# Performance work log

Measured on AMD Instinct MI355X. Metric: run time of the kernel, lower is better.

The kernel has to match this reference:

```python
import jax, jax.numpy as jnp
import numpy as np

LATENT = 128   # latent_size
FDIM = 32      # feature_dim per plane
FSIZE = 512    # feature_size -> grid is (FSIZE+1)^2
HID = 256      # hidden_dim
N = 500000     # number of query points
IN_DIM = 3
G = FSIZE + 1
SDF_IN = 3 * FDIM + LATENT + IN_DIM  # 227


def setup_inputs() -> dict:
    key = jax.random.key(0)
    ks = jax.random.split(key, 6)
    x = jax.random.normal(ks[0], (N, LATENT + IN_DIM), jnp.float32)
    # 3 tri-planes, each [FDIM, G, G], init randn*0.01 as in FeaturePlanes
    P = jax.random.normal(ks[1], (3, FDIM, G, G), jnp.float32) * 0.01

    def lin(k, fan_in, fan_out):
        s = 1.0 / np.sqrt(fan_in)
        kw, kb = jax.random.split(k)
        W = jax.random.uniform(kw, (fan_in, fan_out), jnp.float32, -s, s)
        b = jax.random.uniform(kb, (fan_out,), jnp.float32, -s, s)
        return W, b

    W0, b0 = lin(ks[2], SDF_IN, HID)
    W1, b1 = lin(ks[3], HID, HID)
    W2, b2 = lin(ks[4], HID, 1)
    return dict(x=x, P=P, W0=W0, b0=b0, W1=W1, b1=b1, W2=W2, b2=b2)


def _sample_plane(plane, uv):
    """Bilinear grid_sample, align_corners=True, padding_mode='border'.
    plane: [C, G, G]; uv: [Npts, 2] with uv[:,0]->width(x), uv[:,1]->height(y).
    Returns [Npts, C]."""
    g = jnp.clip((uv + 1.0) * 0.5 * (G - 1), 0.0, G - 1)  # unnormalize + border clamp
    gx, gy = g[:, 0], g[:, 1]
    x0f, y0f = jnp.floor(gx), jnp.floor(gy)
    x0 = x0f.astype(jnp.int32)
    y0 = y0f.astype(jnp.int32)
    x1 = jnp.minimum(x0 + 1, G - 1)
    y1 = jnp.minimum(y0 + 1, G - 1)
    wx = gx - x0f
    wy = gy - y0f
    v00 = plane[:, y0, x0]  # [C, Npts]
    v01 = plane[:, y0, x1]
    v10 = plane[:, y1, x0]
    v11 = plane[:, y1, x1]
    top = v00 * (1.0 - wx) + v01 * wx
    bot = v10 * (1.0 - wx) + v11 * wx
    return (top * (1.0 - wy) + bot * wy).T  # [Npts, C]


def reference(x, P, W0, b0, W1, b1, W2, b2):
    in_latents = x[:, :LATENT]
    in_x = x[:, -3:]
    coords = jax.lax.stop_gradient(in_x)  # matches .detach() before grid_sample
    # dimension pairs (0,1), (0,2), (1,2) -> one bilinear lookup each, vmapped
    uv = jnp.stack([coords[:, [0, 1]], coords[:, [0, 2]], coords[:, [1, 2]]])  # [3,N,2]
    feats = jax.vmap(_sample_plane)(P, uv)              # [3, N, FDIM]
    feats = jnp.transpose(feats, (1, 0, 2)).reshape(x.shape[0], 3 * FDIM)
    net_in = jnp.concatenate([in_latents, in_x, feats], axis=-1)  # [N, 227]
    h = jax.nn.relu(net_in @ W0 + b0)
    h = jax.nn.relu(h @ W1 + b1)
    out = (h @ W2 + b2).squeeze(-1)  # [N]
    return out
```

## Files before the change

kernel.cpp:

```cpp
#include <hip/hip_runtime.h>
#include <stdint.h>

#define XDIM 131
#define GSZ 513
#define TROWS 64
#define SC_OFF 32768

typedef __attribute__((ext_vector_type(8))) short bf16x8;
typedef __attribute__((ext_vector_type(4))) float f32x4;
typedef unsigned int uint32;

__device__ __forceinline__ uint32 pk2bf(float a, float b) {
  uint32 r;
  asm volatile("v_cvt_pk_bf16_f32 %0, %1, %2" : "=v"(r) : "v"(a), "v"(b));
  return r;
}
__device__ __forceinline__ unsigned short f2bf(float f) {
  return (unsigned short)pk2bf(f, f);
}
__device__ __forceinline__ float bf2f(unsigned short s) {
  return __uint_as_float(((uint32)s) << 16);
}
__device__ __forceinline__ int slot16(int r) { return (r * 16) ^ (((r >> 3) & 1) << 5); }

__global__ void prep_pt(const float* __restrict__ P, unsigned short* __restrict__ Pt) {
  int i = blockIdx.x * 256 + threadIdx.x;
  const int CELLS = 3 * GSZ * GSZ;
  if (i >= CELLS) return;
  int pl = i / (GSZ * GSZ);
  int yx = i - pl * (GSZ * GSZ);
  const float* src = P + (size_t)pl * 32 * GSZ * GSZ + yx;
  const size_t GG = (size_t)GSZ * GSZ;
  uint4* dst = (uint4*)(Pt + (size_t)i * 32);
#pragma unroll
  for (int w = 0; w < 4; ++w) {
    uint4 t;
    t.x = pk2bf(src[(w * 8 + 0) * GG], src[(w * 8 + 1) * GG]);
    t.y = pk2bf(src[(w * 8 + 2) * GG], src[(w * 8 + 3) * GG]);
    t.z = pk2bf(src[(w * 8 + 4) * GG], src[(w * 8 + 5) * GG]);
    t.w = pk2bf(src[(w * 8 + 6) * GG], src[(w * 8 + 7) * GG]);
    dst[w] = t;
  }
}

__global__ void prep_w(const float* __restrict__ W0, const float* __restrict__ W1,
                       unsigned short* __restrict__ W0g, unsigned short* __restrict__ W1g) {
  int i = blockIdx.x * 256 + threadIdx.x;
  int sel = i >> 13;
  int t = i & 8191;
  int kb = t >> 10;
  int g  = (t >> 8) & 3;
  int n  = t & 255;
  float vv[8];
#pragma unroll
  for (int j = 0; j < 8; ++j) {
    int k = kb * 32 + g * 8 + j;
    float val;
    if (sel == 0) {
      int src = (k < 131) ? k : ((k >= 136 && k < 232) ? k - 5 : -1);
      val = (src >= 0) ? W0[src * 256 + n] : 0.f;
    } else {
      val = W1[k * 256 + n];
    }
    vv[j] = val;
  }
  uint4 o;
  o.x = pk2bf(vv[0], vv[1]);
  o.y = pk2bf(vv[2], vv[3]);
  o.z = pk2bf(vv[4], vv[5]);
  o.w = pk2bf(vv[6], vv[7]);
  unsigned short* dst = (sel == 0 ? W0g : W1g) + (size_t)t * 8;
  *(uint4*)dst = o;
}

__global__ __launch_bounds__(256) void k_gather(
    const float* __restrict__ x, const unsigned short* __restrict__ Pt,
    unsigned short* __restrict__ feats, int Npts)
{
  int idx = blockIdx.x * 256 + threadIdx.x;
  int p = min(idx >> 2, Npts - 1);
  int q = idx & 3;
  const float* xr = x + (size_t)p * XDIM + 128;
  float cc0 = xr[0], cc1 = xr[1], cc2 = xr[2];

  const unsigned short* pp[12];
  float w[12];
#pragma unroll
  for (int pl = 0; pl < 3; ++pl) {
    float u = (pl == 2) ? cc1 : cc0;
    float v = (pl == 0) ? cc1 : cc2;
    float gx = fminf(fmaxf((u + 1.f) * 256.f, 0.f), 512.f);
    float gy = fminf(fmaxf((v + 1.f) * 256.f, 0.f), 512.f);
    float x0f = floorf(gx), y0f = floorf(gy);
    int x0 = (int)x0f, y0 = (int)y0f;
    int x1 = min(x0 + 1, GSZ - 1), y1 = min(y0 + 1, GSZ - 1);
    float wx = gx - x0f, wy = gy - y0f;
    w[pl * 4 + 0] = (1.f - wx) * (1.f - wy);
    w[pl * 4 + 1] = wx * (1.f - wy);
    w[pl * 4 + 2] = (1.f - wx) * wy;
    w[pl * 4 + 3] = wx * wy;
    const unsigned short* pb = Pt + (size_t)pl * GSZ * GSZ * 32 + q * 8;
    pp[pl * 4 + 0] = pb + (size_t)(y0 * GSZ + x0) * 32;
    pp[pl * 4 + 1] = pb + (size_t)(y0 * GSZ + x1) * 32;
    pp[pl * 4 + 2] = pb + (size_t)(y1 * GSZ + x0) * 32;
    pp[pl * 4 + 3] = pb + (size_t)(y1 * GSZ + x1) * 32;
  }
  bf16x8 v[12];
#pragma unroll
  for (int j = 0; j < 12; ++j) v[j] = *(const bf16x8*)pp[j];

#pragma unroll
  for (int pl = 0; pl < 3; ++pl) {
    float f[8];
#pragma unroll
    for (int j = 0; j < 8; ++j) {
      f[j] = w[pl * 4 + 0] * bf2f((unsigned short)v[pl * 4 + 0][j])
           + w[pl * 4 + 1] * bf2f((unsigned short)v[pl * 4 + 1][j])
           + w[pl * 4 + 2] * bf2f((unsigned short)v[pl * 4 + 2][j])
           + w[pl * 4 + 3] * bf2f((unsigned short)v[pl * 4 + 3][j]);
    }
    uint4 fv;
    fv.x = pk2bf(f[0], f[1]);
    fv.y = pk2bf(f[2], f[3]);
    fv.z = pk2bf(f[4], f[5]);
    fv.w = pk2bf(f[6], f[7]);
    *(uint4*)(feats + (size_t)p * 96 + pl * 32 + q * 8) = fv;
  }
}

__device__ __forceinline__ void gemm64(const unsigned char* __restrict__ lds_,
                                       const unsigned short* __restrict__ Wg,
                                       int cg, int lr, int lg, f32x4 (&acc)[4][4])
{
#pragma unroll
  for (int kb = 0; kb < 8; ++kb) {
    bf16x8 a[4];
    const unsigned char* ab = lds_ + (kb * 4 + lg) * 1024;
#pragma unroll
    for (int mf = 0; mf < 4; ++mf)
      a[mf] = *(const bf16x8*)(ab + slot16(mf * 16 + lr));
    const unsigned short* wb = Wg + ((size_t)(kb * 4 + lg) * 256 + cg * 64 + lr) * 8;
    __builtin_amdgcn_s_setprio(1);
#pragma unroll
    for (int nf = 0; nf < 4; ++nf) {
      bf16x8 b = *(const bf16x8*)(wb + nf * 128);
#pragma unroll
      for (int mf = 0; mf < 4; ++mf)
        acc[mf][nf] = __builtin_amdgcn_mfma_f32_16x16x32_bf16(a[mf], b, acc[mf][nf], 0, 0, 0);
    }
    __builtin_amdgcn_s_setprio(0);
  }
}

template<int MODE>
__global__ __launch_bounds__(256, 4) void sdf_mlp(
    const float* __restrict__ x, const float* __restrict__ P,
    const unsigned short* __restrict__ Pt, const unsigned short* __restrict__ feats,
    const unsigned short* __restrict__ W0g, const unsigned short* __restrict__ W1g,
    const float* __restrict__ b0, const float* __restrict__ b1,
    const float* __restrict__ W2, const float* __restrict__ b2v,
    float* __restrict__ out, int Npts)
{
  __shared__ __align__(16) unsigned char lds[SC_OFF + 1024];

  const int tid = threadIdx.x;
  const int p0 = blockIdx.x * TROWS;
  const int lane = tid & 63, cg = tid >> 6;
  const int lr = lane & 15, lg = lane >> 4;

#pragma unroll
  for (int i = 0; i < 4; ++i) {
    int t = i * 256 + tid;
    int cb = t & 15, r = t >> 4;
    int p = min(p0 + r, Npts - 1);
    const float* src = x + (size_t)p * XDIM + cb * 8;
    uint4 v;
    v.x = pk2bf(src[0], src[1]);
    v.y = pk2bf(src[2], src[3]);
    v.z = pk2bf(src[4], src[5]);
    v.w = pk2bf(src[6], src[7]);
    *(uint4*)(lds + cb * 1024 + slot16(r)) = v;
  }
  if (tid < 64) {
    int p = min(p0 + tid, Npts - 1);
    const float* xr = x + (size_t)p * XDIM + 128;
    uint4 v;
    v.x = pk2bf(xr[0], xr[1]);
    v.y = pk2bf(xr[2], 0.f);
    v.z = 0u; v.w = 0u;
    *(uint4*)(lds + 16 * 1024 + slot16(tid)) = v;
  } else {
    uint4 z = {0u, 0u, 0u, 0u};
    ((uint4*)(lds + 29 * 1024))[tid - 64] = z;
  }

  if (MODE == 0) {
#pragma unroll
    for (int i = 0; i < 3; ++i) {
      int t = i * 256 + tid;
      int r = t & 63, j = t >> 6;
      int p = min(p0 + r, Npts - 1);
      uint4 fv = *(const uint4*)(feats + (size_t)p * 96 + j * 8);
      *(uint4*)(lds + (17 + j) * 1024 + slot16(r)) = fv;
    }
  } else {
    int p_l = tid >> 2, q = tid & 3;
    int p = min(p0 + p_l, Npts - 1);
    const float* xr = x + (size_t)p * XDIM + 128;
    float cc0 = xr[0], cc1 = xr[1], cc2 = xr[2];
#pragma unroll
    for (int pl = 0; pl < 3; ++pl) {
      float u = (pl == 2) ? cc1 : cc0;
      float v = (pl == 0) ? cc1 : cc2;
      float gx = fminf(fmaxf((u + 1.f) * 256.f, 0.f), 512.f);
      float gy = fminf(fmaxf((v + 1.f) * 256.f, 0.f), 512.f);
      float x0f = floorf(gx), y0f = floorf(gy);
      int x0 = (int)x0f, y0 = (int)y0f;
      int x1 = min(x0 + 1, GSZ - 1), y1 = min(y0 + 1, GSZ - 1);
      float wx = gx - x0f, wy = gy - y0f;
      float w00 = (1.f - wx) * (1.f - wy), w01 = wx * (1.f - wy);
      float w10 = (1.f - wx) * wy,        w11 = wx * wy;
      float f[8];
      if (MODE == 1) {
        const unsigned short* pb = Pt + (size_t)pl * GSZ * GSZ * 32 + q * 8;
        bf16x8 v00 = *(const bf16x8*)(pb + (size_t)(y0 * GSZ + x0) * 32);
        bf16x8 v01 = *(const bf16x8*)(pb + (size_t)(y0 * GSZ + x1) * 32);
        bf16x8 v10 = *(const bf16x8*)(pb + (size_t)(y1 * GSZ + x0) * 32);
        bf16x8 v11 = *(const bf16x8*)(pb + (size_t)(y1 * GSZ + x1) * 32);
#pragma unroll
        for (int j = 0; j < 8; ++j) {
          f[j] = w00 * bf2f((unsigned short)v00[j]) + w01 * bf2f((unsigned short)v01[j])
               + w10 * bf2f((unsigned short)v10[j]) + w11 * bf2f((unsigned short)v11[j]);
        }
      } else {
#pragma unroll
        for (int j = 0; j < 8; ++j) {
          const float* pc = P + (size_t)(pl * 32 + q * 8 + j) * GSZ * GSZ;
          f[j] = w00 * pc[y0 * GSZ + x0] + w01 * pc[y0 * GSZ + x1]
               + w10 * pc[y1 * GSZ + x0] + w11 * pc[y1 * GSZ + x1];
        }
      }
      uint4 fv;
      fv.x = pk2bf(f[0], f[1]);
      fv.y = pk2bf(f[2], f[3]);
      fv.z = pk2bf(f[4], f[5]);
      fv.w = pk2bf(f[6], f[7]);
      *(uint4*)(lds + (17 + pl * 4 + q) * 1024 + slot16(p_l)) = fv;
    }
  }
  __syncthreads();

  {
    f32x4 acc[4][4];
#pragma unroll
    for (int mf = 0; mf < 4; ++mf)
#pragma unroll
      for (int nf = 0; nf < 4; ++nf) acc[mf][nf] = (f32x4){0.f, 0.f, 0.f, 0.f};
    gemm64(lds, W0g, cg, lr, lg, acc);
    __syncthreads();
#pragma unroll
    for (int nf = 0; nf < 4; ++nf) {
      int col = cg * 64 + nf * 16 + lr;
      float bs = b0[col];
      unsigned char* base = lds + (col >> 3) * 1024 + (col & 7) * 2;
#pragma unroll
      for (int mf = 0; mf < 4; ++mf)
#pragma unroll
        for (int reg = 0; reg < 4; ++reg) {
          int row = mf * 16 + lg * 4 + reg;
          *(unsigned short*)(base + slot16(row)) = f2bf(fmaxf(acc[mf][nf][reg] + bs, 0.f));
        }
    }
  }
  __syncthreads();

  {
    f32x4 acc[4][4];
#pragma unroll
    for (int mf = 0; mf < 4; ++mf)
#pragma unroll
      for (int nf = 0; nf < 4; ++nf) acc[mf][nf] = (f32x4){0.f, 0.f, 0.f, 0.f};
    gemm64(lds, W1g, cg, lr, lg, acc);

    float part[4][4];
#pragma unroll
    for (int mf = 0; mf < 4; ++mf)
#pragma unroll
      for (int reg = 0; reg < 4; ++reg) part[mf][reg] = 0.f;
#pragma unroll
    for (int nf = 0; nf < 4; ++nf) {
      int col = cg * 64 + nf * 16 + lr;
      float bs = b1[col];
      float w2v = W2[col];
#pragma unroll
      for (int mf = 0; mf < 4; ++mf)
#pragma unroll
        for (int reg = 0; reg < 4; ++reg)
          part[mf][reg] += fmaxf(acc[mf][nf][reg] + bs, 0.f) * w2v;
    }
#pragma unroll
    for (int mf = 0; mf < 4; ++mf)
#pragma unroll
      for (int reg = 0; reg < 4; ++reg) {
        float v = part[mf][reg];
        v += __shfl_xor(v, 1);
        v += __shfl_xor(v, 2);
        v += __shfl_xor(v, 4);
        v += __shfl_xor(v, 8);
        part[mf][reg] = v;
      }
    if (lr == 0) {
      float* sc = (float*)(lds + SC_OFF) + cg * 64;
#pragma unroll
      for (int mf = 0; mf < 4; ++mf) {
        float4 pv;
        pv.x = part[mf][0]; pv.y = part[mf][1]; pv.z = part[mf][2]; pv.w = part[mf][3];
        *(float4*)(sc + mf * 16 + lg * 4) = pv;
      }
    }
  }
  __syncthreads();
  if (tid < 64) {
    const float* sc = (const float*)(lds + SC_OFF);
    float s = sc[tid] + sc[64 + tid] + sc[128 + tid] + sc[192 + tid] + b2v[0];
    int p = p0 + tid;
    if (p < Npts) out[p] = s;
  }
}

extern "C" void kernel_launch(void* const* d_in, const int* in_sizes, int n_in,
                              void* d_out, int out_size, void* d_ws, size_t ws_size,
                              hipStream_t stream)
{
  const float* x  = (const float*)d_in[0];
  const float* P  = (const float*)d_in[1];
  const float* W0 = (const float*)d_in[2];
  const float* b0 = (const float*)d_in[3];
  const float* W1 = (const float*)d_in[4];
  const float* b1 = (const float*)d_in[5];
  const float* W2 = (const float*)d_in[6];
  const float* b2 = (const float*)d_in[7];
  float* out = (float*)d_out;
  int Npts = in_sizes[0] / XDIM;

  const size_t PT_BYTES = (size_t)3 * GSZ * GSZ * 32 * 2;
  const size_t WG_BYTES = (size_t)8192 * 8 * 2;
  const size_t FT_BYTES = (size_t)Npts * 96 * 2;
  char* ws = (char*)d_ws;

  int mode;
  unsigned short *Ptb = nullptr, *W0g, *W1g, *ft = nullptr;
  if (ws_size >= PT_BYTES + 2 * WG_BYTES + FT_BYTES) {
    mode = 0;
    Ptb = (unsigned short*)ws;
    W0g = (unsigned short*)(ws + PT_BYTES);
    W1g = (unsigned short*)(ws + PT_BYTES + WG_BYTES);
    ft  = (unsigned short*)(ws + PT_BYTES + 2 * WG_BYTES);
  } else if (ws_size >= PT_BYTES + 2 * WG_BYTES) {
    mode = 1;
    Ptb = (unsigned short*)ws;
    W0g = (unsigned short*)(ws + PT_BYTES);
    W1g = (unsigned short*)(ws + PT_BYTES + WG_BYTES);
  } else {
    mode = 2;
    W0g = (unsigned short*)ws;
    W1g = (unsigned short*)(ws + WG_BYTES);
  }

  prep_w<<<64, 256, 0, stream>>>(W0, W1, W0g, W1g);
  if (mode != 2) prep_pt<<<(3 * GSZ * GSZ + 255) / 256, 256, 0, stream>>>(P, Ptb);
  if (mode == 0) k_gather<<<(Npts * 4 + 255) / 256, 256, 0, stream>>>(x, Ptb, ft, Npts);

  int nblk = (Npts + TROWS - 1) / TROWS;
  if (mode == 0)
    sdf_mlp<0><<<nblk, 256, 0, stream>>>(x, P, Ptb, ft, W0g, W1g, b0, b1, W2, b2, out, Npts);
  else if (mode == 1)
    sdf_mlp<1><<<nblk, 256, 0, stream>>>(x, P, Ptb, ft, W0g, W1g, b0, b1, W2, b2, out, Npts);
  else
    sdf_mlp<2><<<nblk, 256, 0, stream>>>(x, P, Ptb, ft, W0g, W1g, b0, b1, W2, b2, out, Npts);
}
```

Baseline: 363.5 us.

## Pre-pack full bf16 input tiles and run a 128-row MLP kernel

Adds a prep kernel that converts each 128-point tile (latents, coords and bilinear tri-plane features) into a bf16, LDS-swizzled 64KB tile in workspace. A new MLP kernel then streams each tile straight into LDS with global_load_lds and runs both GEMMs over 128 rows per block, with MFMA priority hints. The aim is to remove per-block fp32 x conversion and gather work from the MLP kernel and to double weight reuse per block. In exchange it needs a larger workspace (with fallbacks to the old paths) and one extra full write and read of the packed activations.

New measurement: 689.4 us. 1.9x slower.

```diff
diff --git a/kernel.cpp b/kernel.cpp
--- a/kernel.cpp
+++ b/kernel.cpp
@@ -5,6 +5,9 @@
 #define GSZ 513
 #define TROWS 64
 #define SC_OFF 32768
+#define BROWS 128
+#define KBS 2048
+#define TILE_BYTES 65536
 
 typedef __attribute__((ext_vector_type(8))) short bf16x8;
 typedef __attribute__((ext_vector_type(4))) float f32x4;
@@ -22,6 +25,12 @@
   return __uint_as_float(((uint32)s) << 16);
 }
 __device__ __forceinline__ int slot16(int r) { return (r * 16) ^ (((r >> 3) & 1) << 5); }
+
+__device__ __forceinline__ void gload_lds16(const void* g, void* l) {
+  __builtin_amdgcn_global_load_lds(
+      (const __attribute__((address_space(1))) uint32*)g,
+      (__attribute__((address_space(3))) uint32*)l, 16, 0, 0);
+}
 
 __global__ void prep_pt(const float* __restrict__ P, unsigned short* __restrict__ Pt) {
   int i = blockIdx.x * 256 + threadIdx.x;
@@ -73,18 +82,38 @@
   *(uint4*)dst = o;
 }
 
-__global__ __launch_bounds__(256) void k_gather(
+__global__ __launch_bounds__(512) void k_prep(
     const float* __restrict__ x, const unsigned short* __restrict__ Pt,
-    unsigned short* __restrict__ feats, int Npts)
-{
-  int idx = blockIdx.x * 256 + threadIdx.x;
-  int p = min(idx >> 2, Npts - 1);
-  int q = idx & 3;
-  const float* xr = x + (size_t)p * XDIM + 128;
-  float cc0 = xr[0], cc1 = xr[1], cc2 = xr[2];
-
-  const unsigned short* pp[12];
-  float w[12];
+    unsigned short* __restrict__ xall, int Npts)
+{
+  const int tid = threadIdx.x;
+  const int p_l = tid >> 2, q = tid & 3;
+  const int p = min(blockIdx.x * BROWS + p_l, Npts - 1);
+  unsigned char* dst = (unsigned char*)xall + (size_t)blockIdx.x * TILE_BYTES;
+  const float* xrow = x + (size_t)p * XDIM;
+  const int sl = slot16(p_l);
+
+#pragma unroll
+  for (int i = 0; i < 4; ++i) {
+    const float* s = xrow + q * 32 + i * 8;
+    uint4 v;
+    v.x = pk2bf(s[0], s[1]);
+    v.y = pk2bf(s[2], s[3]);
+    v.z = pk2bf(s[4], s[5]);
+    v.w = pk2bf(s[6], s[7]);
+    *(uint4*)(dst + (q * 4 + i) * KBS + sl) = v;
+  }
+  float cc0 = xrow[128], cc1 = xrow[129], cc2 = xrow[130];
+  if (q == 0) {
+    uint4 v;
+    v.x = pk2bf(cc0, cc1);
+    v.y = pk2bf(cc2, 0.f);
+    v.z = 0u; v.w = 0u;
+    *(uint4*)(dst + 16 * KBS + sl) = v;
+  } else {
+    uint4 z = {0u, 0u, 0u, 0u};
+    *(uint4*)(dst + (28 + q) * KBS + sl) = z;
+  }
 #pragma unroll
   for (int pl = 0; pl < 3; ++pl) {
     float u = (pl == 2) ? cc1 : cc0;
@@ -95,29 +124,195 @@
     int x0 = (int)x0f, y0 = (int)y0f;
     int x1 = min(x0 + 1, GSZ - 1), y1 = min(y0 + 1, GSZ - 1);
     float wx = gx - x0f, wy = gy - y0f;
-    w[pl * 4 + 0] = (1.f - wx) * (1.f - wy);
-    w[pl * 4 + 1] = wx * (1.f - wy);
-    w[pl * 4 + 2] = (1.f - wx) * wy;
-    w[pl * 4 + 3] = wx * wy;
+    float w00 = (1.f - wx) * (1.f - wy), w01 = wx * (1.f - wy);
+    float w10 = (1.f - wx) * wy,        w11 = wx * wy;
     const unsigned short* pb = Pt + (size_t)pl * GSZ * GSZ * 32 + q * 8;
-    pp[pl * 4 + 0] = pb + (size_t)(y0 * GSZ + x0) * 32;
-    pp[pl * 4 + 1] = pb + (size_t)(y0 * GSZ + x1) * 32;
-    pp[pl * 4 + 2] = pb + (size_t)(y1 * GSZ + x0) * 32;
-    pp[pl * 4 + 3] = pb + (size_t)(y1 * GSZ + x1) * 32;
-  }
-  bf16x8 v[12];
-#pragma unroll
-  for (int j = 0; j < 12; ++j) v[j] = *(const bf16x8*)pp[j];
-
+    bf16x8 v00 = *(const bf16x8*)(pb + (size_t)(y0 * GSZ + x0) * 32);
+    bf16x8 v01 = *(const bf16x8*)(pb + (size_t)(y0 * GSZ + x1) * 32);
+    bf16x8 v10 = *(const bf16x8*)(pb + (size_t)(y1 * GSZ + x0) * 32);
+    bf16x8 v11 = *(const bf16x8*)(pb + (size_t)(y1 * GSZ + x1) * 32);
+    float f[8];
+#pragma unroll
+    for (int j = 0; j < 8; ++j) {
+      f[j] = w00 * bf2f((unsigned short)v00[j]) + w01 * bf2f((unsigned short)v01[j])
+           + w10 * bf2f((unsigned short)v10[j]) + w11 * bf2f((unsigned short)v11[j]);
+    }
+    uint4 fv;
+    fv.x = pk2bf(f[0], f[1]);
+    fv.y = pk2bf(f[2], f[3]);
+    fv.z = pk2bf(f[4], f[5]);
+    fv.w = pk2bf(f[6], f[7]);
+    *(uint4*)(dst + (17 + pl * 4 + q) * KBS + sl) = fv;
+  }
+}
+
+__device__ __forceinline__ void gemm128(const unsigned char* __restrict__ lds_,
+                                        const unsigned short* __restrict__ Wg,
+                                        int cg, int lr, int lg, f32x4 (&acc)[8][4])
+{
+#pragma unroll
+  for (int kb = 0; kb < 8; ++kb) {
+    const unsigned char* ab = lds_ + (kb * 4 + lg) * KBS;
+    const unsigned short* wb = Wg + ((size_t)(kb * 4 + lg) * 256 + cg * 64 + lr) * 8;
+    bf16x8 b[4];
+#pragma unroll
+    for (int nf = 0; nf < 4; ++nf) b[nf] = *(const bf16x8*)(wb + nf * 128);
+    bf16x8 a[4];
+#pragma unroll
+    for (int mf = 0; mf < 4; ++mf) a[mf] = *(const bf16x8*)(ab + slot16(mf * 16 + lr));
+    __builtin_amdgcn_s_setprio(1);
+#pragma unroll
+    for (int nf = 0; nf < 4; ++nf)
+#pragma unroll
+      for (int mf = 0; mf < 4; ++mf)
+        acc[mf][nf] = __builtin_amdgcn_mfma_f32_16x16x32_bf16(a[mf], b[nf], acc[mf][nf], 0, 0, 0);
+    __builtin_amdgcn_s_setprio(0);
+#pragma unroll
+    for (int mf = 0; mf < 4; ++mf) a[mf] = *(const bf16x8*)(ab + slot16(64 + mf * 16 + lr));
+    __builtin_amdgcn_s_setprio(1);
+#pragma unroll
+    for (int nf = 0; nf < 4; ++nf)
+#pragma unroll
+      for (int mf = 0; mf < 4; ++mf)
+        acc[4 + mf][nf] = __builtin_amdgcn_mfma_f32_16x16x32_bf16(a[mf], b[nf], acc[4 + mf][nf], 0, 0, 0);
+    __builtin_amdgcn_s_setprio(0);
+  }
+}
+
+__global__ __launch_bounds__(256, 2) void sdf_big(
+    const unsigned short* __restrict__ xall,
+    const unsigned short* __restrict__ W0g, const unsigned short* __restrict__ W1g,
+    const float* __restrict__ b0, const float* __restrict__ b1,
+    const float* __restrict__ W2, const float* __restrict__ b2v,
+    float* __restrict__ out, int Npts)
+{
+  __shared__ __align__(16) unsigned char lds[TILE_BYTES + 2048];
+
+  const int tid = threadIdx.x;
+  const int lane = tid & 63, cg = tid >> 6;
+  const int lr = lane & 15, lg = lane >> 4;
+
+  {
+    const unsigned char* src = (const unsigned char*)xall
+                             + (size_t)blockIdx.x * TILE_BYTES + lane * 16;
+#pragma unroll
+    for (int i = 0; i < 16; ++i) {
+      int chunk = cg * 16 + i;
+      gload_lds16(src + chunk * 1024, lds + chunk * 1024);
+    }
+    asm volatile("s_waitcnt vmcnt(0)" ::: "memory");
+  }
+  __syncthreads();
+
+  {
+    f32x4 acc[8][4];
+#pragma unroll
+    for (int mh = 0; mh < 8; ++mh)
+#pragma unroll
+      for (int nf = 0; nf < 4; ++nf) acc[mh][nf] = (f32x4){0.f, 0.f, 0.f, 0.f};
+    gemm128(lds, W0g, cg, lr, lg, acc);
+    __syncthreads();
+#pragma unroll
+    for (int nf = 0; nf < 4; ++nf) {
+      int col = cg * 64 + nf * 16 + lr;
+      float bs = b0[col];
+      unsigned char* base = lds + (col >> 3) * KBS + (col & 7) * 2;
+#pragma unroll
+      for (int mh = 0; mh < 8; ++mh)
+#pragma unroll
+        for (int reg = 0; reg < 4; ++reg) {
+          int row = mh * 16 + lg * 4 + reg;
+          *(unsigned short*)(base + slot16(row)) = f2bf(fmaxf(acc[mh][nf][reg] + bs, 0.f));
+        }
+    }
+  }
+  __syncthreads();
+
+  {
+    f32x4 acc[8][4];
+#pragma unroll
+    for (int mh = 0; mh < 8; ++mh)
+#pragma unroll
+      for (int nf = 0; nf < 4; ++nf) acc[mh][nf] = (f32x4){0.f, 0.f, 0.f, 0.f};
+    gemm128(lds, W1g, cg, lr, lg, acc);
+
+    float part[8][4];
+#pragma unroll
+    for (int mh = 0; mh < 8; ++mh)
+#pragma unroll
+      for (int reg = 0; reg < 4; ++reg) part[mh][reg] = 0.f;
+#pragma unroll
+    for (int nf = 0; nf < 4; ++nf) {
+      int col = cg * 64 + nf * 16 + lr;
+      float bs = b1[col];
+      float w2v = W2[col];
+#pragma unroll
+      for (int mh = 0; mh < 8; ++mh)
+#pragma unroll
+        for (int reg = 0; reg < 4; ++reg)
+          part[mh][reg] += fmaxf(acc[mh][nf][reg] + bs, 0.f) * w2v;
+    }
+#pragma unroll
+    for (int mh = 0; mh < 8; ++mh)
+#pragma unroll
+      for (int reg = 0; reg < 4; ++reg) {
+        float v = part[mh][reg];
+        v += __shfl_xor(v, 1);
+        v += __shfl_xor(v, 2);
+        v += __shfl_xor(v, 4);
+        v += __shfl_xor(v, 8);
+        part[mh][reg] = v;
+      }
+    if (lr == 0) {
+      float* sc = (float*)(lds + TILE_BYTES) + cg * 128;
+#pragma unroll
+      for (int mh = 0; mh < 8; ++mh) {
+        float4 pv;
+        pv.x = part[mh][0]; pv.y = part[mh][1]; pv.z = part[mh][2]; pv.w = part[mh][3];
+        *(float4*)(sc + mh * 16 + lg * 4) = pv;
+      }
+    }
+  }
+  __syncthreads();
+  if (tid < 128) {
+    const float* sc = (const float*)(lds + TILE_BYTES);
+    float s = sc[tid] + sc[128 + tid] + sc[256 + tid] + sc[384 + tid] + b2v[0];
+    int p = blockIdx.x * BROWS + tid;
+    if (p < Npts) out[p] = s;
+  }
+}
+
+__global__ __launch_bounds__(256) void k_gather(
+    const float* __restrict__ x, const unsigned short* __restrict__ Pt,
+    unsigned short* __restrict__ feats, int Npts)
+{
+  int idx = blockIdx.x * 256 + threadIdx.x;
+  int p = min(idx >> 2, Npts - 1);
+  int q = idx & 3;
+  const float* xr = x + (size_t)p * XDIM + 128;
+  float cc0 = xr[0], cc1 = xr[1], cc2 = xr[2];
 #pragma unroll
   for (int pl = 0; pl < 3; ++pl) {
+    float u = (pl == 2) ? cc1 : cc0;
+    float v = (pl == 0) ? cc1 : cc2;
+    float gx = fminf(fmaxf((u + 1.f) * 256.f, 0.f), 512.f);
+    float gy = fminf(fmaxf((v + 1.f) * 256.f, 0.f), 512.f);
+    float x0f = floorf(gx), y0f = floorf(gy);
+    int x0 = (int)x0f, y0 = (int)y0f;
+    int x1 = min(x0 + 1, GSZ - 1), y1 = min(y0 + 1, GSZ - 1);
+    float wx = gx - x0f, wy = gy - y0f;
+    float w00 = (1.f - wx) * (1.f - wy), w01 = wx * (1.f - wy);
+    float w10 = (1.f - wx) * wy,        w11 = wx * wy;
+    const unsigned short* pb = Pt + (size_t)pl * GSZ * GSZ * 32 + q * 8;
+    bf16x8 v00 = *(const bf16x8*)(pb + (size_t)(y0 * GSZ + x0) * 32);
+    bf16x8 v01 = *(const bf16x8*)(pb + (size_t)(y0 * GSZ + x1) * 32);
+    bf16x8 v10 = *(const bf16x8*)(pb + (size_t)(y1 * GSZ + x0) * 32);
+    bf16x8 v11 = *(const bf16x8*)(pb + (size_t)(y1 * GSZ + x1) * 32);
     float f[8];
 #pragma unroll
     for (int j = 0; j < 8; ++j) {
-      f[j] = w[pl * 4 + 0] * bf2f((unsigned short)v[pl * 4 + 0][j])
-           + w[pl * 4 + 1] * bf2f((unsigned short)v[pl * 4 + 1][j])
-           + w[pl * 4 + 2] * bf2f((unsigned short)v[pl * 4 + 2][j])
-           + w[pl * 4 + 3] * bf2f((unsigned short)v[pl * 4 + 3][j]);
+      f[j] = w00 * bf2f((unsigned short)v00[j]) + w01 * bf2f((unsigned short)v01[j])
+           + w10 * bf2f((unsigned short)v10[j]) + w11 * bf2f((unsigned short)v11[j]);
     }
     uint4 fv;
     fv.x = pk2bf(f[0], f[1]);
@@ -342,40 +537,54 @@
   const float* b2 = (const float*)d_in[7];
   float* out = (float*)d_out;
   int Npts = in_sizes[0] / XDIM;
+  int nt_big = (Npts + BROWS - 1) / BROWS;
 
   const size_t PT_BYTES = (size_t)3 * GSZ * GSZ * 32 * 2;
   const size_t WG_BYTES = (size_t)8192 * 8 * 2;
+  const size_t XA_BYTES = (size_t)nt_big * TILE_BYTES;
   const size_t FT_BYTES = (size_t)Npts * 96 * 2;
   char* ws = (char*)d_ws;
 
   int mode;
-  unsigned short *Ptb = nullptr, *W0g, *W1g, *ft = nullptr;
-  if (ws_size >= PT_BYTES + 2 * WG_BYTES + FT_BYTES) {
+  unsigned short *Ptb = nullptr, *W0g, *W1g, *ext = nullptr;
+  if (ws_size >= PT_BYTES + 2 * WG_BYTES + XA_BYTES) {
     mode = 0;
     Ptb = (unsigned short*)ws;
     W0g = (unsigned short*)(ws + PT_BYTES);
     W1g = (unsigned short*)(ws + PT_BYTES + WG_BYTES);
-    ft  = (unsigned short*)(ws + PT_BYTES + 2 * WG_BYTES);
-  } else if (ws_size >= PT_BYTES + 2 * WG_BYTES) {
+    ext = (unsigned short*)(ws + PT_BYTES + 2 * WG_BYTES);
+  } else if (ws_size >= PT_BYTES + 2 * WG_BYTES + FT_BYTES) {
     mode = 1;
     Ptb = (unsigned short*)ws;
     W0g = (unsigned short*)(ws + PT_BYTES);
     W1g = (unsigned short*)(ws + PT_BYTES + WG_BYTES);
+    ext = (unsigned short*)(ws + PT_BYTES + 2 * WG_BYTES);
+  } else if (ws_size >= PT_BYTES + 2 * WG_BYTES) {
+    mode = 2;
+    Ptb = (unsigned short*)ws;
+    W0g = (unsigned short*)(ws + PT_BYTES);
+    W1g = (unsigned short*)(ws + PT_BYTES + WG_BYTES);
   } else {
-    mode = 2;
+    mode = 3;
     W0g = (unsigned short*)ws;
     W1g = (unsigned short*)(ws + WG_BYTES);
   }
 
   prep_w<<<64, 256, 0, stream>>>(W0, W1, W0g, W1g);
-  if (mode != 2) prep_pt<<<(3 * GSZ * GSZ + 255) / 256, 256, 0, stream>>>(P, Ptb);
-  if (mode == 0) k_gather<<<(Npts * 4 + 255) / 256, 256, 0, stream>>>(x, Ptb, ft, Npts);
-
-  int nblk = (Npts + TROWS - 1) / TROWS;
-  if (mode == 0)
-    sdf_mlp<0><<<nblk, 256, 0, stream>>>(x, P, Ptb, ft, W0g, W1g, b0, b1, W2, b2, out, Npts);
-  else if (mode == 1)
-    sdf_mlp<1><<<nblk, 256, 0, stream>>>(x, P, Ptb, ft, W0g, W1g, b0, b1, W2, b2, out, Npts);
-  else
-    sdf_mlp<2><<<nblk, 256, 0, stream>>>(x, P, Ptb, ft, W0g, W1g, b0, b1, W2, b2, out, Npts);
-}
+  if (mode != 3) prep_pt<<<(3 * GSZ * GSZ + 255) / 256, 256, 0, stream>>>(P, Ptb);
+
+  if (mode == 0) {
+    k_prep<<<nt_big, 512, 0, stream>>>(x, Ptb, ext, Npts);
+    sdf_big<<<nt_big, 256, 0, stream>>>(ext, W0g, W1g, b0, b1, W2, b2, out, Npts);
+  } else {
+    int nblk = (Npts + TROWS - 1) / TROWS;
+    if (mode == 1) {
+      k_gather<<<(Npts * 4 + 255) / 256, 256, 0, stream>>>(x, Ptb, ext, Npts);
+      sdf_mlp<0><<<nblk, 256, 0, stream>>>(x, P, Ptb, ext, W0g, W1g, b0, b1, W2, b2, out, Npts);
+    } else if (mode == 2) {
+      sdf_mlp<1><<<nblk, 256, 0, stream>>>(x, P, Ptb, nullptr, W0g, W1g, b0, b1, W2, b2, out, Npts);
+    } else {
+      sdf_mlp<2><<<nblk, 256, 0, stream>>>(x, P, Ptb, nullptr, W0g, W1g, b0, b1, W2, b2, out, Npts);
+    }
+  }
+}
```
